# Kernel tuning notes

Hardware: AMD Instinct MI355X
Metric: run time of the kernel (lower is better)

Reference implementation:

```python
import jax, jax.numpy as jnp
import numpy as np

NUM_CLUSTERS = 256


def setup_inputs() -> dict:
    key = jax.random.key(0)
    k1, k2, k3 = jax.random.split(key, 3)
    a, b, k = 8192, 8192, NUM_CLUSTERS
    w_mat = jax.random.uniform(k1, (a, b), dtype=jnp.float32)
    # softmax-like assignment probabilities over clusters
    p_l = jax.nn.softmax(jax.random.normal(k2, (a, k), dtype=jnp.float32), axis=-1)
    p_r = jax.nn.softmax(jax.random.normal(k3, (b, k), dtype=jnp.float32), axis=-1)
    clusters_p = jnp.ones((k,), dtype=jnp.float32) / k  # uniform init as in module
    return {"w_mat": w_mat, "p_l": p_l, "p_r": p_r, "clusters_p": clusters_p}


def reference(w_mat, p_l, p_r, clusters_p):
    # Algebraically equivalent to:
    #   ((w[:,:,None] * (p_l[:,None,:] + p_r[None,:,:] - 2*p_l[:,None,:]*p_r[None,:,:]))
    #      .sum((0,1)) / clusters_p).sum()
    # without materializing the (a,b,k) tensor.
    row_w = jnp.sum(w_mat, axis=1)            # (a,)  sum_b w[a,b]
    col_w = jnp.sum(w_mat, axis=0)            # (b,)  sum_a w[a,b]
    rs = row_w @ p_l                           # (k,)  sum_{a,b} w * p_l
    cs = col_w @ p_r                           # (k,)  sum_{a,b} w * p_r
    # cross[k] = sum_{a,b} p_l[a,k] * w[a,b] * p_r[b,k]
    cross = jnp.einsum("ka,ak->k", p_l.T @ w_mat, p_r)  # (k,)
    return jnp.sum((rs + cs - 2.0 * cross) / clusters_p)
```

## Files before the change

kernel.cpp:

```cpp
#include <hip/hip_runtime.h>
#include <stdint.h>

#define A_DIM 8192
#define B_DIM 8192
#define K_CL  256
#define BM    64
#define BK    64
#define NSLAB 4
#define SLABW (B_DIM / NSLAB)
#define NKS   (SLABW / BK)

typedef short bf16x8 __attribute__((ext_vector_type(8)));
typedef float f32x4  __attribute__((ext_vector_type(4)));
typedef unsigned short u16;

__device__ __forceinline__ u16 f2bf(float f) {
    unsigned int u = __float_as_uint(f);
    u += 0x7fffu + ((u >> 16) & 1u);
    return (u16)(u >> 16);
}

__global__ __launch_bounds__(256) void k_prep(const float* __restrict__ pr,
                                              const float* __restrict__ pl,
                                              const float* __restrict__ cp,
                                              u16* __restrict__ Bpack,
                                              float* __restrict__ pl_dot,
                                              float* __restrict__ out) {
    const int t = threadIdx.x;
    if (blockIdx.x < 256) {
        const int kb = blockIdx.x;
        const int lane = t & 63, wv = t >> 6;
        const int lg = lane >> 4, l15 = lane & 15;
#pragma unroll
        for (int ci = 0; ci < 4; ci++) {
            const int c = wv * 4 + ci;
            float v[8];
#pragma unroll
            for (int j = 0; j < 8; j++)
                v[j] = pr[(size_t)(kb * 32 + lg * 8 + j) * K_CL + c * 16 + l15];
            union { bf16x8 b; unsigned int u[4]; } o;
#pragma unroll
            for (int j = 0; j < 4; j++)
                o.u[j] = (unsigned int)f2bf(v[2 * j]) | ((unsigned int)f2bf(v[2 * j + 1]) << 16);
            *(bf16x8*)(Bpack + ((size_t)(kb * 16 + c) * 64 + lane) * 8) = o.b;
        }
    } else {
        if (blockIdx.x == 256 && t == 0) out[0] = 0.0f;
        const int row0 = (blockIdx.x - 256) * 32;
        const int r = t >> 3, sub = t & 7;
        const float* prow = pl + (size_t)(row0 + r) * K_CL + sub * 32;
        const float* cpr = cp + sub * 32;
        float v = 0.f;
#pragma unroll
        for (int q = 0; q < 8; q++) {
            float4 x = *(const float4*)(prow + q * 4);
            float4 c = *(const float4*)(cpr + q * 4);
            v += x.x / c.x + x.y / c.y + x.z / c.z + x.w / c.w;
        }
        v += __shfl_xor(v, 1, 64);
        v += __shfl_xor(v, 2, 64);
        v += __shfl_xor(v, 4, 64);
        if (sub == 0) pl_dot[row0 + r] = v;
    }
}

__global__ __launch_bounds__(256, 2) void k_main(const float* __restrict__ w,
                                                 const float* __restrict__ pl,
                                                 const u16* __restrict__ Bpack,
                                                 const float* __restrict__ cp,
                                                 const float* __restrict__ pl_dot,
                                                 float* __restrict__ out) {
    __shared__ float Abuf[4][BM * BK];
    __shared__ float pld_s[BM];
    __shared__ float red[4];

    const int bid = blockIdx.x;
    const int slab = bid & 3;
    const int m0 = (bid >> 2) * BM;
    const int tid = threadIdx.x;
    const int lane = tid & 63, wv = tid >> 6;
    const int lg = lane >> 4, l15 = lane & 15;

    if (tid < BM) pld_s[tid] = pl_dot[m0 + tid];

    float rcp_cp[4];
#pragma unroll
    for (int ni = 0; ni < 4; ni++)
        rcp_cp[ni] = 1.0f / cp[wv * 64 + ni * 16 + l15];

    __syncthreads();
    float pld[4];
#pragma unroll
    for (int mi = 0; mi < 4; mi++) pld[mi] = pld_s[mi * 16 + l15];

    const char* wbase = (const char*)(w + (size_t)m0 * B_DIM + (size_t)slab * SLABW);

    auto stage = [&](int buf, int ks) {
#pragma unroll
        for (int i = 0; i < 4; i++) {
            const int row_local = wv * 16 + i * 4 + lg;
            const int sw = (row_local & 7) << 4;
            const char* src = wbase + (size_t)row_local * (B_DIM * 4) + ks * 256 + ((l15 * 16) ^ sw);
            void* dst = (void*)&Abuf[buf][(wv * 16 + i * 4) * BK];
            __builtin_amdgcn_global_load_lds(
                (const __attribute__((address_space(1))) void*)src,
                (__attribute__((address_space(3))) void*)dst, 16, 0, 0);
        }
    };

    const u16* bslab = Bpack + (size_t)slab * 64 * 8192;

#define LOADB(arr, ks) do {                                                          \
        const u16* bp_ = bslab + (size_t)(ks) * 2 * 8192;                            \
        _Pragma("unroll")                                                            \
        for (int ni_ = 0; ni_ < 4; ni_++)                                            \
            arr[ni_] = *(const bf16x8*)(bp_ + (size_t)(wv * 4 + ni_) * 512 + lane * 8); \
        _Pragma("unroll")                                                            \
        for (int ni_ = 0; ni_ < 4; ni_++)                                            \
            arr[4 + ni_] = *(const bf16x8*)(bp_ + (size_t)(16 + wv * 4 + ni_) * 512 + lane * 8); \
    } while (0)

#define COMPUTE(cur, arr) do {                                                       \
        const char* abase_ = (const char*)&Abuf[(cur)][0];                           \
        _Pragma("unroll")                                                            \
        for (int h_ = 0; h_ < 2; h_++) {                                             \
            _Pragma("unroll")                                                        \
            for (int mi_ = 0; mi_ < 4; mi_++) {                                      \
                const int row_ = mi_ * 16 + l15;                                     \
                const int sw_ = (row_ & 7) << 4;                                     \
                const char* rp_ = abase_ + row_ * 256;                               \
                f32x4 f0_ = *(const f32x4*)(rp_ + ((h_ * 128 + lg * 32) ^ sw_));     \
                f32x4 f1_ = *(const f32x4*)(rp_ + ((h_ * 128 + lg * 32 + 16) ^ sw_));\
                if (wv == 0)                                                         \
                    sums[mi_] += f0_[0]+f0_[1]+f0_[2]+f0_[3]+f1_[0]+f1_[1]+f1_[2]+f1_[3]; \
                union { bf16x8 v; unsigned int u[4]; } a_;                           \
                a_.u[0] = __builtin_amdgcn_perm(__float_as_uint(f0_[1]), __float_as_uint(f0_[0]), 0x07060302u); \
                a_.u[1] = __builtin_amdgcn_perm(__float_as_uint(f0_[3]), __float_as_uint(f0_[2]), 0x07060302u); \
                a_.u[2] = __builtin_amdgcn_perm(__float_as_uint(f1_[1]), __float_as_uint(f1_[0]), 0x07060302u); \
                a_.u[3] = __builtin_amdgcn_perm(__float_as_uint(f1_[3]), __float_as_uint(f1_[2]), 0x07060302u); \
                _Pragma("unroll")                                                    \
                for (int ni_ = 0; ni_ < 4; ni_++)                                    \
                    acc[mi_][ni_] = __builtin_amdgcn_mfma_f32_16x16x32_bf16(         \
                        a_.v, (arr)[h_ * 4 + ni_], acc[mi_][ni_], 0, 0, 0);          \
            }                                                                        \
        }                                                                            \
    } while (0)

#define BODY(ks, WAITN, BCUR, BNXT, DOSTAGE, DOLOADB) do {                           \
        asm volatile("s_waitcnt vmcnt(" #WAITN ")" ::: "memory");                    \
        __builtin_amdgcn_s_barrier();                                                \
        __builtin_amdgcn_sched_barrier(0);                                           \
        if (DOLOADB) LOADB(BNXT, (ks) + 1);                                          \
        if (DOSTAGE) stage(((ks) + 3) & 3, (ks) + 3);                                \
        COMPUTE((ks) & 3, BCUR);                                                     \
    } while (0)

    f32x4 acc[4][4];
#pragma unroll
    for (int mi = 0; mi < 4; mi++)
#pragma unroll
        for (int ni = 0; ni < 4; ni++) {
            f32x4 z = {0.f, 0.f, 0.f, 0.f};
            acc[mi][ni] = z;
        }
    float sums[4] = {0.f, 0.f, 0.f, 0.f};

    bf16x8 bA[8], bB[8];
    stage(0, 0); stage(1, 1); stage(2, 2);
    LOADB(bA, 0);

    for (int ks = 0; ks < NKS - 4; ks += 2) {
        BODY(ks,     16, bA, bB, 1, 1);
        BODY(ks + 1, 16, bB, bA, 1, 1);
    }
    BODY(28, 16, bA, bB, 1, 1);
    BODY(29, 16, bB, bA, 0, 1);
    BODY(30, 12, bA, bB, 0, 1);
    BODY(31,  8, bB, bA, 0, 0);

#undef BODY
#undef COMPUTE
#undef LOADB

    float tot = 0.f;
    if (wv == 0) {
#pragma unroll
        for (int mi = 0; mi < 4; mi++) tot += sums[mi] * pld[mi];
    }
#pragma unroll
    for (int mi = 0; mi < 4; mi++) {
#pragma unroll
        for (int r = 0; r < 4; r++) {
            const float* plrow = pl + (size_t)(m0 + mi * 16 + lg * 4 + r) * K_CL + wv * 64 + l15;
#pragma unroll
            for (int ni = 0; ni < 4; ni++)
                tot += acc[mi][ni][r] * (1.0f - 2.0f * plrow[ni * 16]) * rcp_cp[ni];
        }
    }
    for (int o = 32; o; o >>= 1) tot += __shfl_down(tot, o, 64);
    if (lane == 0) red[wv] = tot;
    __syncthreads();
    if (tid == 0) atomicAdd(out, red[0] + red[1] + red[2] + red[3]);
}

extern "C" void kernel_launch(void* const* d_in, const int* in_sizes, int n_in,
                              void* d_out, int out_size, void* d_ws, size_t ws_size,
                              hipStream_t stream) {
    const float* w  = (const float*)d_in[0];
    const float* pl = (const float*)d_in[1];
    const float* pr = (const float*)d_in[2];
    const float* cp = (const float*)d_in[3];
    float* out = (float*)d_out;

    u16* Bpack = (u16*)d_ws;
    float* pl_dot = (float*)((char*)d_ws + (size_t)4 * 1024 * 1024);

    k_prep<<<dim3(512), dim3(256), 0, stream>>>(pr, pl, cp, Bpack, pl_dot, out);
    k_main<<<dim3(128 * NSLAB), dim3(256), 0, stream>>>(w, pl, Bpack, cp, pl_dot, out);
}
```

Before: 72.62 us.

## Switch main GEMM to 32x32x16 MFMA and fold row-sum term into epilogue

Replaces the 16x16x32 bf16 MFMA tiling with 32x32x16 MFMAs (each wave owning 64 rows by 64 clusters), repacking p_r in prep to match the new B fragment layout. The separate pl_dot precomputation is removed. Row sums of w are now split across all four waves and combined through shared-memory atomics, then applied per element in the epilogue as p*rowsum/cp. The goal is fewer MFMA issues, fewer LDS reads per FLOP, and a lighter prep kernel, at the cost of a different LDS swizzle/staging layout, more epilogue global loads of p_l, and an added barrier.

```diff
diff --git a/kernel.cpp b/kernel.cpp
--- a/kernel.cpp
+++ b/kernel.cpp
@@ -12,6 +12,7 @@
 
 typedef short bf16x8 __attribute__((ext_vector_type(8)));
 typedef float f32x4  __attribute__((ext_vector_type(4)));
+typedef float f32x16 __attribute__((ext_vector_type(16)));
 typedef unsigned short u16;
 
 __device__ __forceinline__ u16 f2bf(float f) {
@@ -21,46 +22,25 @@
 }
 
 __global__ __launch_bounds__(256) void k_prep(const float* __restrict__ pr,
-                                              const float* __restrict__ pl,
-                                              const float* __restrict__ cp,
                                               u16* __restrict__ Bpack,
-                                              float* __restrict__ pl_dot,
                                               float* __restrict__ out) {
+    const int kb2 = blockIdx.x;
     const int t = threadIdx.x;
-    if (blockIdx.x < 256) {
-        const int kb = blockIdx.x;
-        const int lane = t & 63, wv = t >> 6;
-        const int lg = lane >> 4, l15 = lane & 15;
-#pragma unroll
-        for (int ci = 0; ci < 4; ci++) {
-            const int c = wv * 4 + ci;
-            float v[8];
-#pragma unroll
-            for (int j = 0; j < 8; j++)
-                v[j] = pr[(size_t)(kb * 32 + lg * 8 + j) * K_CL + c * 16 + l15];
-            union { bf16x8 b; unsigned int u[4]; } o;
-#pragma unroll
-            for (int j = 0; j < 4; j++)
-                o.u[j] = (unsigned int)f2bf(v[2 * j]) | ((unsigned int)f2bf(v[2 * j + 1]) << 16);
-            *(bf16x8*)(Bpack + ((size_t)(kb * 16 + c) * 64 + lane) * 8) = o.b;
-        }
-    } else {
-        if (blockIdx.x == 256 && t == 0) out[0] = 0.0f;
-        const int row0 = (blockIdx.x - 256) * 32;
-        const int r = t >> 3, sub = t & 7;
-        const float* prow = pl + (size_t)(row0 + r) * K_CL + sub * 32;
-        const float* cpr = cp + sub * 32;
-        float v = 0.f;
-#pragma unroll
-        for (int q = 0; q < 8; q++) {
-            float4 x = *(const float4*)(prow + q * 4);
-            float4 c = *(const float4*)(cpr + q * 4);
-            v += x.x / c.x + x.y / c.y + x.z / c.z + x.w / c.w;
-        }
-        v += __shfl_xor(v, 1, 64);
-        v += __shfl_xor(v, 2, 64);
-        v += __shfl_xor(v, 4, 64);
-        if (sub == 0) pl_dot[row0 + r] = v;
+    if (kb2 == 0 && t == 0) out[0] = 0.0f;
+    const int lane = t & 63, wv = t >> 6;
+    const int l31 = lane & 31, half = lane >> 5;
+#pragma unroll
+    for (int ci = 0; ci < 2; ci++) {
+        const int c2 = wv * 2 + ci;
+        float v[8];
+#pragma unroll
+        for (int j = 0; j < 8; j++)
+            v[j] = pr[(size_t)(kb2 * 16 + half * 8 + j) * K_CL + c2 * 32 + l31];
+        union { bf16x8 b; unsigned int u[4]; } o;
+#pragma unroll
+        for (int j = 0; j < 4; j++)
+            o.u[j] = (unsigned int)f2bf(v[2 * j]) | ((unsigned int)f2bf(v[2 * j + 1]) << 16);
+        *(bf16x8*)(Bpack + ((size_t)(kb2 * 8 + c2) * 64 + lane) * 8) = o.b;
     }
 }
 
@@ -68,10 +48,9 @@
                                                  const float* __restrict__ pl,
                                                  const u16* __restrict__ Bpack,
                                                  const float* __restrict__ cp,
-                                                 const float* __restrict__ pl_dot,
                                                  float* __restrict__ out) {
     __shared__ float Abuf[4][BM * BK];
-    __shared__ float pld_s[BM];
+    __shared__ float rowsum[BM];
     __shared__ float red[4];
 
     const int bid = blockIdx.x;
@@ -79,91 +58,89 @@
     const int m0 = (bid >> 2) * BM;
     const int tid = threadIdx.x;
     const int lane = tid & 63, wv = tid >> 6;
-    const int lg = lane >> 4, l15 = lane & 15;
-
-    if (tid < BM) pld_s[tid] = pl_dot[m0 + tid];
-
-    float rcp_cp[4];
-#pragma unroll
-    for (int ni = 0; ni < 4; ni++)
-        rcp_cp[ni] = 1.0f / cp[wv * 64 + ni * 16 + l15];
+    const int l31 = lane & 31, half = lane >> 5;
+    const int kb2base = slab * 128;
+
+    if (tid < BM) rowsum[tid] = 0.0f;
+
+    float rcp_cp[2];
+#pragma unroll
+    for (int n2 = 0; n2 < 2; n2++)
+        rcp_cp[n2] = 1.0f / cp[wv * 64 + n2 * 32 + l31];
 
     __syncthreads();
-    float pld[4];
-#pragma unroll
-    for (int mi = 0; mi < 4; mi++) pld[mi] = pld_s[mi * 16 + l15];
 
     const char* wbase = (const char*)(w + (size_t)m0 * B_DIM + (size_t)slab * SLABW);
 
     auto stage = [&](int buf, int ks) {
 #pragma unroll
         for (int i = 0; i < 4; i++) {
-            const int row_local = wv * 16 + i * 4 + lg;
-            const int sw = (row_local & 7) << 4;
-            const char* src = wbase + (size_t)row_local * (B_DIM * 4) + ks * 256 + ((l15 * 16) ^ sw);
-            void* dst = (void*)&Abuf[buf][(wv * 16 + i * 4) * BK];
+            const int r4 = tid >> 4;
+            const int sw = r4 << 4;
+            const char* src = wbase + (size_t)(i * 16 + r4) * (B_DIM * 4) + ks * 256 + (((tid & 15) * 16) ^ sw);
+            void* dst = (void*)&Abuf[buf][i * 1024 + (tid >> 4) * 64 + (tid & 15) * 4];
             __builtin_amdgcn_global_load_lds(
                 (const __attribute__((address_space(1))) void*)src,
                 (__attribute__((address_space(3))) void*)dst, 16, 0, 0);
         }
     };
 
-    const u16* bslab = Bpack + (size_t)slab * 64 * 8192;
-
-#define LOADB(arr, ks) do {                                                          \
-        const u16* bp_ = bslab + (size_t)(ks) * 2 * 8192;                            \
-        _Pragma("unroll")                                                            \
-        for (int ni_ = 0; ni_ < 4; ni_++)                                            \
-            arr[ni_] = *(const bf16x8*)(bp_ + (size_t)(wv * 4 + ni_) * 512 + lane * 8); \
-        _Pragma("unroll")                                                            \
-        for (int ni_ = 0; ni_ < 4; ni_++)                                            \
-            arr[4 + ni_] = *(const bf16x8*)(bp_ + (size_t)(16 + wv * 4 + ni_) * 512 + lane * 8); \
+#define LOADB(arr, ks) do {                                                              \
+        _Pragma("unroll")                                                                \
+        for (int kf_ = 0; kf_ < 4; kf_++)                                                \
+            _Pragma("unroll")                                                            \
+            for (int n2_ = 0; n2_ < 2; n2_++)                                            \
+                (arr)[kf_ * 2 + n2_] = *(const bf16x8*)(Bpack +                          \
+                    (((size_t)(kb2base + (ks) * 4 + kf_) * 8 + wv * 2 + n2_) * 64 + lane) * 8); \
     } while (0)
 
-#define COMPUTE(cur, arr) do {                                                       \
-        const char* abase_ = (const char*)&Abuf[(cur)][0];                           \
-        _Pragma("unroll")                                                            \
-        for (int h_ = 0; h_ < 2; h_++) {                                             \
-            _Pragma("unroll")                                                        \
-            for (int mi_ = 0; mi_ < 4; mi_++) {                                      \
-                const int row_ = mi_ * 16 + l15;                                     \
-                const int sw_ = (row_ & 7) << 4;                                     \
-                const char* rp_ = abase_ + row_ * 256;                               \
-                f32x4 f0_ = *(const f32x4*)(rp_ + ((h_ * 128 + lg * 32) ^ sw_));     \
-                f32x4 f1_ = *(const f32x4*)(rp_ + ((h_ * 128 + lg * 32 + 16) ^ sw_));\
-                if (wv == 0)                                                         \
-                    sums[mi_] += f0_[0]+f0_[1]+f0_[2]+f0_[3]+f1_[0]+f1_[1]+f1_[2]+f1_[3]; \
-                union { bf16x8 v; unsigned int u[4]; } a_;                           \
-                a_.u[0] = __builtin_amdgcn_perm(__float_as_uint(f0_[1]), __float_as_uint(f0_[0]), 0x07060302u); \
-                a_.u[1] = __builtin_amdgcn_perm(__float_as_uint(f0_[3]), __float_as_uint(f0_[2]), 0x07060302u); \
-                a_.u[2] = __builtin_amdgcn_perm(__float_as_uint(f1_[1]), __float_as_uint(f1_[0]), 0x07060302u); \
-                a_.u[3] = __builtin_amdgcn_perm(__float_as_uint(f1_[3]), __float_as_uint(f1_[2]), 0x07060302u); \
-                _Pragma("unroll")                                                    \
-                for (int ni_ = 0; ni_ < 4; ni_++)                                    \
-                    acc[mi_][ni_] = __builtin_amdgcn_mfma_f32_16x16x32_bf16(         \
-                        a_.v, (arr)[h_ * 4 + ni_], acc[mi_][ni_], 0, 0, 0);          \
-            }                                                                        \
-        }                                                                            \
+#define COMPUTE(cur, arr) do {                                                           \
+        const char* abase_ = (const char*)&Abuf[(cur)][0];                               \
+        const int sw_ = (l31 & 15) << 4;                                                 \
+        _Pragma("unroll")                                                                \
+        for (int kf_ = 0; kf_ < 4; kf_++) {                                              \
+            bf16x8 a_[2];                                                                \
+            f32x4 f0_[2], f1_[2];                                                        \
+            _Pragma("unroll")                                                            \
+            for (int mf_ = 0; mf_ < 2; mf_++) {                                          \
+                const char* rp_ = abase_ + (mf_ * 32 + l31) * 256;                       \
+                f0_[mf_] = *(const f32x4*)(rp_ + ((kf_ * 64 + half * 32) ^ sw_));        \
+                f1_[mf_] = *(const f32x4*)(rp_ + ((kf_ * 64 + half * 32 + 16) ^ sw_));   \
+                union { bf16x8 v; unsigned int u[4]; } pa_;                              \
+                pa_.u[0] = __builtin_amdgcn_perm(__float_as_uint(f0_[mf_][1]), __float_as_uint(f0_[mf_][0]), 0x07060302u); \
+                pa_.u[1] = __builtin_amdgcn_perm(__float_as_uint(f0_[mf_][3]), __float_as_uint(f0_[mf_][2]), 0x07060302u); \
+                pa_.u[2] = __builtin_amdgcn_perm(__float_as_uint(f1_[mf_][1]), __float_as_uint(f1_[mf_][0]), 0x07060302u); \
+                pa_.u[3] = __builtin_amdgcn_perm(__float_as_uint(f1_[mf_][3]), __float_as_uint(f1_[mf_][2]), 0x07060302u); \
+                a_[mf_] = pa_.v;                                                         \
+            }                                                                            \
+            if (kf_ == wv) {                \
+                sums0 += f0_[0][0]+f0_[0][1]+f0_[0][2]+f0_[0][3]+f1_[0][0]+f1_[0][1]+f1_[0][2]+f1_[0][3]; \
+                sums1 += f0_[1][0]+f0_[1][1]+f0_[1][2]+f0_[1][3]+f1_[1][0]+f1_[1][1]+f1_[1][2]+f1_[1][3]; \
+            }                                                                            \
+            _Pragma("unroll")                                                            \
+            for (int mf_ = 0; mf_ < 2; mf_++)                                            \
+                _Pragma("unroll")                                                        \
+                for (int n2_ = 0; n2_ < 2; n2_++)                                        \
+                    acc[mf_ * 2 + n2_] = __builtin_amdgcn_mfma_f32_32x32x16_bf16(        \
+                        a_[mf_], (arr)[kf_ * 2 + n2_], acc[mf_ * 2 + n2_], 0, 0, 0);     \
+        }                                                                                \
     } while (0)
 
-#define BODY(ks, WAITN, BCUR, BNXT, DOSTAGE, DOLOADB) do {                           \
-        asm volatile("s_waitcnt vmcnt(" #WAITN ")" ::: "memory");                    \
-        __builtin_amdgcn_s_barrier();                                                \
-        __builtin_amdgcn_sched_barrier(0);                                           \
-        if (DOLOADB) LOADB(BNXT, (ks) + 1);                                          \
-        if (DOSTAGE) stage(((ks) + 3) & 3, (ks) + 3);                                \
-        COMPUTE((ks) & 3, BCUR);                                                     \
+#define BODY(ks, WAITN, BCUR, BNXT, DOSTAGE, DOLOADB) do {                               \
+        asm volatile("s_waitcnt vmcnt(" #WAITN ")" ::: "memory");                        \
+        __builtin_amdgcn_s_barrier();                                                    \
+        __builtin_amdgcn_sched_barrier(0);                                               \
+        if (DOLOADB) LOADB(BNXT, (ks) + 1);                                              \
+        if (DOSTAGE) stage(((ks) + 3) & 3, (ks) + 3);                                    \
+        COMPUTE((ks) & 3, BCUR);                                                         \
     } while (0)
 
-    f32x4 acc[4][4];
-#pragma unroll
-    for (int mi = 0; mi < 4; mi++)
-#pragma unroll
-        for (int ni = 0; ni < 4; ni++) {
-            f32x4 z = {0.f, 0.f, 0.f, 0.f};
-            acc[mi][ni] = z;
-        }
-    float sums[4] = {0.f, 0.f, 0.f, 0.f};
+    f32x16 acc[4];
+#pragma unroll
+    for (int i = 0; i < 4; i++)
+#pragma unroll
+        for (int r = 0; r < 16; r++) acc[i][r] = 0.f;
+    float sums0 = 0.f, sums1 = 0.f;
 
     bf16x8 bA[8], bB[8];
     stage(0, 0); stage(1, 1); stage(2, 2);
@@ -182,19 +159,30 @@
 #undef COMPUTE
 #undef LOADB
 
+    {
+        float v0 = sums0 + __shfl_xor(sums0, 32, 64);
+        float v1 = sums1 + __shfl_xor(sums1, 32, 64);
+        if (lane < 32) {
+            atomicAdd(&rowsum[l31], v0);
+            atomicAdd(&rowsum[32 + l31], v1);
+        }
+    }
+    __syncthreads();
+
     float tot = 0.f;
-    if (wv == 0) {
-#pragma unroll
-        for (int mi = 0; mi < 4; mi++) tot += sums[mi] * pld[mi];
-    }
-#pragma unroll
-    for (int mi = 0; mi < 4; mi++) {
-#pragma unroll
-        for (int r = 0; r < 4; r++) {
-            const float* plrow = pl + (size_t)(m0 + mi * 16 + lg * 4 + r) * K_CL + wv * 64 + l15;
-#pragma unroll
-            for (int ni = 0; ni < 4; ni++)
-                tot += acc[mi][ni][r] * (1.0f - 2.0f * plrow[ni * 16]) * rcp_cp[ni];
+#pragma unroll
+    for (int mf = 0; mf < 2; mf++) {
+#pragma unroll
+        for (int reg = 0; reg < 16; reg++) {
+            const int lrow = mf * 32 + (reg & 3) + 8 * (reg >> 2) + 4 * half;
+            const float rs = rowsum[lrow];
+            const float* plrow = pl + (size_t)(m0 + lrow) * K_CL + wv * 64 + l31;
+#pragma unroll
+            for (int n2 = 0; n2 < 2; n2++) {
+                const float q = acc[mf * 2 + n2][reg];
+                const float p = plrow[n2 * 32];
+                tot += (q + p * (rs - 2.0f * q)) * rcp_cp[n2];
+            }
         }
     }
     for (int o = 32; o; o >>= 1) tot += __shfl_down(tot, o, 64);
@@ -213,8 +201,7 @@
     float* out = (float*)d_out;
 
     u16* Bpack = (u16*)d_ws;
-    float* pl_dot = (float*)((char*)d_ws + (size_t)4 * 1024 * 1024);
-
-    k_prep<<<dim3(512), dim3(256), 0, stream>>>(pr, pl, cp, Bpack, pl_dot, out);
-    k_main<<<dim3(128 * NSLAB), dim3(256), 0, stream>>>(w, pl, Bpack, cp, pl_dot, out);
-}
+
+    k_prep<<<dim3(512), dim3(256), 0, stream>>>(pr, Bpack, out);
+    k_main<<<dim3(128 * NSLAB), dim3(256), 0, stream>>>(w, pl, Bpack, cp, out);
+}
```

Result: slower. 74.83 us (+3.0%).
